# Performance work log

Hardware: AMD Instinct MI355X
Metric: run time of the kernel (lower is better)

The kernel has to match this reference:

```python
import jax, jax.numpy as jnp
import numpy as np

NUM_ENTITIES = 64
PAD, BOS, EOS = 0, 1, 2
B, S = 512, 512


def setup_inputs() -> dict:
    key = jax.random.key(0)
    k1, k2, k3 = jax.random.split(key, 3)
    emissions = jax.random.normal(k1, (B, S, NUM_ENTITIES), dtype=jnp.float32)
    entities = jax.random.randint(k2, (B, S), 0, NUM_ENTITIES)
    mask = jnp.ones((B, S), dtype=bool)
    # transitions param, initialized as in _init_transitions
    t = jax.random.uniform(k3, (NUM_ENTITIES, NUM_ENTITIES), jnp.float32, -0.1, 0.1)
    t = t.at[:, BOS].set(-10000.0)
    t = t.at[EOS, :].set(-10000.0)
    t = t.at[PAD, :].set(-10000.0)
    t = t.at[:, PAD].set(-10000.0)
    t = t.at[PAD, PAD].set(0.0)
    t = t.at[PAD, EOS].set(0.0)
    return {"emissions": emissions, "transitions": t, "entities": entities, "mask": mask}


def _crf_nll(emissions, transitions, entities, mask):
    mf = mask.astype(emissions.dtype)  # [B,S]
    # ---- gold path score (vectorized over time) ----
    first = entities[:, 0]
    last_idx = jnp.sum(mask.astype(jnp.int32), axis=1) - 1  # [B]
    last = jnp.take_along_axis(entities, last_idx[:, None], axis=1)[:, 0]
    e = jnp.take_along_axis(emissions, entities[:, :, None], axis=2)[:, :, 0]  # [B,S]
    t = transitions[entities[:, :-1], entities[:, 1:]]  # [B,S-1]
    score = (transitions[BOS, first] + e[:, 0]
             + jnp.sum((e[:, 1:] + t) * mf[:, 1:], axis=1)
             + transitions[last, EOS])  # [B]
    # ---- log partition via scan over time ----
    alpha0 = transitions[BOS][None, :] + emissions[:, 0]  # [B,E]

    def step(alpha, xs):
        em_t, m_t = xs  # [B,E], [B] bool
        # scores[b, prev, cur] = alpha[b,prev] + T[prev,cur] + em[b,cur]
        scores = alpha[:, :, None] + transitions[None, :, :] + em_t[:, None, :]
        new_alpha = jax.nn.logsumexp(scores, axis=1)  # [B,E]
        alpha = jnp.where(m_t[:, None], new_alpha, alpha)
        return alpha, None

    alpha, _ = jax.lax.scan(step, alpha0,
                            (jnp.swapaxes(emissions[:, 1:], 0, 1), mask[:, 1:].T))
    log_z = jax.nn.logsumexp(alpha + transitions[:, EOS][None, :], axis=1)  # [B]
    return -jnp.mean(score - log_z)


def reference(emissions, transitions, entities, mask):
    return _crf_nll(emissions, transitions, entities, mask)
```

## Files before the change

kernel.cpp:

```cpp
#include <hip/hip_runtime.h>

#define NE 64
#define BB 512
#define SS 512
#define TMID 256
#define NBWD (SS - 1 - TMID)
#define NCHAIN 32
#define BOS_S 1
#define EOS_S 2
#define LN2 0.69314718055994531f
#define DR 8

typedef float f32x4 __attribute__((ext_vector_type(4)));
typedef int   i32x4 __attribute__((ext_vector_type(4)));
typedef short bf16x8 __attribute__((ext_vector_type(8)));

#define WG_SCOPE __HIP_MEMORY_SCOPE_WORKGROUP

__device__ __forceinline__ float wave_sum(float v) {
#pragma unroll
    for (int off = 32; off > 0; off >>= 1)
        v += __shfl_xor(v, off, 64);
    return v;
}

__device__ __forceinline__ unsigned pack2(float lo, float hi) {
    return __builtin_amdgcn_perm(__float_as_uint(hi), __float_as_uint(lo), 0x07060302u);
}

__device__ __forceinline__ unsigned short bf16_rne(float f) {
    unsigned u = __float_as_uint(f);
    return (unsigned short)((u + 0x7fffu + ((u >> 16) & 1u)) >> 16);
}

template <bool FWD>
__device__ __forceinline__ void producer_loop(const float* embase, float (*ring)[1024],
                                              int* ready, int* cons, int p, int lane,
                                              int tmax) {
    int t = 1 + p;
    f32x4 buf[4];
    if (t <= tmax) {
        const float* r = embase + (size_t)(FWD ? t : (SS - t)) * NE;
#pragma unroll
        for (int m = 0; m < 4; ++m) buf[m] = *(const f32x4*)(r + 16 * m);
    }
    while (t <= tmax) {
        int tn = t + 3;
        f32x4 nb[4];
        if (tn <= tmax) {
            const float* r = embase + (size_t)(FWD ? tn : (SS - tn)) * NE;
#pragma unroll
            for (int m = 0; m < 4; ++m) nb[m] = *(const f32x4*)(r + 16 * m);
        }
        while (__hip_atomic_load(cons, __ATOMIC_ACQUIRE, WG_SCOPE) < t - DR)
            __builtin_amdgcn_s_sleep(1);
        int slot = t & (DR - 1);
        f32x4* dst = (f32x4*)ring[slot];
#pragma unroll
        for (int m = 0; m < 4; ++m) {
            f32x4 w;
#pragma unroll
            for (int r2 = 0; r2 < 4; ++r2) w[r2] = __expf(buf[m][r2]);
            dst[m * 64 + lane] = w;
        }
        __hip_atomic_store(&ready[slot], t, __ATOMIC_RELEASE, WG_SCOPE);
#pragma unroll
        for (int m = 0; m < 4; ++m) buf[m] = nb[m];
        t = tn;
    }
}

__global__ __launch_bounds__(512, 1) void crf_fused(const float* __restrict__ em,
                                                    const float* __restrict__ T,
                                                    const int* __restrict__ ent,
                                                    float* __restrict__ out_mean) {
    const int lane = threadIdx.x & 63;
    const int wv = threadIdx.x >> 6;

    if (blockIdx.x >= NCHAIN) {
        const int b = (blockIdx.x - NCHAIN) * 8 + wv;
        const float* emb = em + (size_t)b * SS * NE;
        const int* entb = ent + b * SS;
        float sc = 0.f;
        for (int t = lane; t < SS; t += 64) {
            int et = entb[t];
            sc += emb[t * NE + et];
            sc += (t == 0) ? T[BOS_S * NE + et] : T[entb[t - 1] * NE + et];
            if (t == SS - 1) sc += T[et * NE + EOS_S];
        }
        sc = wave_sum(sc);
        if (lane == 0) atomicAdd(out_mean, -sc * (1.0f / (float)BB));
        return;
    }

    __shared__ float ringf[DR][1024];
    __shared__ float ringb[DR][1024];
    __shared__ int readyf[DR], readyb[DR];
    __shared__ int consf, consb;
    __shared__ float wbuf[1024];
    __shared__ int shiftb_s;
    __shared__ int doneb;

    if (threadIdx.x < DR) { readyf[threadIdx.x] = 0; readyb[threadIdx.x] = 0; }
    if (threadIdx.x == 0) { consf = 0; consb = 0; doneb = 0; }
    __syncthreads();

    const int g = blockIdx.x;
    const int n = lane & 15;
    const int q = lane >> 4;

    if (wv >= 2) {
        const float* embase = em + ((size_t)(g * 16 + n) * SS) * NE + 4 * q;
        if (wv <= 4)
            producer_loop<true>(embase, ringf, readyf, &consf, wv - 2, lane, TMID);
        else
            producer_loop<false>(embase, ringb, readyb, &consb, wv - 5, lane, NBWD);
        return;
    }

#define LOAD_G(RING, READY, BUF, T_)                                             \
    do {                                                                         \
        int _slot = (T_) & (DR - 1);                                             \
        while (__hip_atomic_load(&READY[_slot], __ATOMIC_ACQUIRE, WG_SCOPE) != (T_)) {} \
        const f32x4* _src = (const f32x4*)RING[_slot];                           \
        BUF[0] = _src[0 * 64 + lane];                                            \
        BUF[1] = _src[1 * 64 + lane];                                            \
        BUF[2] = _src[2 * 64 + lane];                                            \
        BUF[3] = _src[3 * 64 + lane];                                            \
    } while (0)

#define STEP_F(T_, GCUR, GNXT, DO_LOAD)                                          \
    do {                                                                         \
        if (DO_LOAD) LOAD_G(ringf, readyf, GNXT, (T_) + 1);                      \
        unsigned u3 = (unsigned)__builtin_amdgcn_readlane(__float_as_int(d[3]), 0); \
        int kk = (int)((u3 >> 23) & 255u) - 127;                                 \
        shift += kk;                                                             \
        float scale = __uint_as_float((unsigned)(127 - kk) << 23);               \
        float ds[16];                                                            \
        _Pragma("unroll") for (int v = 0; v < 16; ++v) ds[v] = d[v] * scale;     \
        i32x4 bi0, bi1;                                                          \
        bi0[0] = (int)pack2(ds[0], ds[1]);   bi0[1] = (int)pack2(ds[2], ds[3]);  \
        bi0[2] = (int)pack2(ds[4], ds[5]);   bi0[3] = (int)pack2(ds[6], ds[7]);  \
        bi1[0] = (int)pack2(ds[8], ds[9]);   bi1[1] = (int)pack2(ds[10], ds[11]);\
        bi1[2] = (int)pack2(ds[12], ds[13]); bi1[3] = (int)pack2(ds[14], ds[15]);\
        bf16x8 B0 = __builtin_bit_cast(bf16x8, bi0);                             \
        bf16x8 B1 = __builtin_bit_cast(bf16x8, bi1);                             \
        _Pragma("unroll") for (int tm = 0; tm < 4; ++tm) {                       \
            f32x4 acc = {0.f, 0.f, 0.f, 0.f};                                    \
            acc = __builtin_amdgcn_mfma_f32_16x16x32_bf16(A[tm][0], B0, acc, 0, 0, 0); \
            acc = __builtin_amdgcn_mfma_f32_16x16x32_bf16(A[tm][1], B1, acc, 0, 0, 0); \
            _Pragma("unroll") for (int r = 0; r < 4; ++r)                        \
                d[4 * tm + r] = acc[r] * GCUR[tm][r];                            \
        }                                                                        \
        asm volatile("" ::: "memory");      \
        if (lane == 0) __hip_atomic_store(&consf, (T_), __ATOMIC_RELAXED, WG_SCOPE); \
    } while (0)

#define STEP_B(T_, GCUR, GNXT, DO_LOAD)                                          \
    do {                                                                         \
        if (DO_LOAD) LOAD_G(ringb, readyb, GNXT, (T_) + 1);                      \
        unsigned u3 = (unsigned)__builtin_amdgcn_readlane(__float_as_int(d[3]), 0); \
        int kk = (int)((u3 >> 23) & 255u) - 127;                                 \
        shift += kk;                                                             \
        float scale = __uint_as_float((unsigned)(127 - kk) << 23);               \
        float ds[16];                                                            \
        _Pragma("unroll") for (int v = 0; v < 16; ++v)                           \
            ds[v] = (d[v] * GCUR[v >> 2][v & 3]) * scale;                        \
        i32x4 bi0, bi1;                                                          \
        bi0[0] = (int)pack2(ds[0], ds[1]);   bi0[1] = (int)pack2(ds[2], ds[3]);  \
        bi0[2] = (int)pack2(ds[4], ds[5]);   bi0[3] = (int)pack2(ds[6], ds[7]);  \
        bi1[0] = (int)pack2(ds[8], ds[9]);   bi1[1] = (int)pack2(ds[10], ds[11]);\
        bi1[2] = (int)pack2(ds[12], ds[13]); bi1[3] = (int)pack2(ds[14], ds[15]);\
        bf16x8 B0 = __builtin_bit_cast(bf16x8, bi0);                             \
        bf16x8 B1 = __builtin_bit_cast(bf16x8, bi1);                             \
        _Pragma("unroll") for (int tm = 0; tm < 4; ++tm) {                       \
            f32x4 acc = {0.f, 0.f, 0.f, 0.f};                                    \
            acc = __builtin_amdgcn_mfma_f32_16x16x32_bf16(A[tm][0], B0, acc, 0, 0, 0); \
            acc = __builtin_amdgcn_mfma_f32_16x16x32_bf16(A[tm][1], B1, acc, 0, 0, 0); \
            _Pragma("unroll") for (int r = 0; r < 4; ++r)                        \
                d[4 * tm + r] = acc[r];                                          \
        }                                                                        \
        asm volatile("" ::: "memory");                                           \
        if (lane == 0) __hip_atomic_store(&consb, (T_), __ATOMIC_RELAXED, WG_SCOPE); \
    } while (0)

    if (wv == 0) {
        const int b = g * 16 + n;

        bf16x8 A[4][2];
#pragma unroll
        for (int tm = 0; tm < 4; ++tm)
#pragma unroll
            for (int kt = 0; kt < 2; ++kt) {
                i32x4 w;
#pragma unroll
                for (int pp = 0; pp < 4; ++pp) {
                    int j0 = 2 * pp, j1 = 2 * pp + 1;
                    int s0 = 16 * (2 * kt + (j0 >> 2)) + 4 * q + (j0 & 3);
                    int s1 = 16 * (2 * kt + (j1 >> 2)) + 4 * q + (j1 & 3);
                    int m = 16 * tm + n;
                    unsigned lo = bf16_rne(__expf(T[s0 * NE + m]));
                    unsigned hi = bf16_rne(__expf(T[s1 * NE + m]));
                    w[pp] = (int)(lo | (hi << 16));
                }
                A[tm][kt] = __builtin_bit_cast(bf16x8, w);
            }

        const float* pe = em + (size_t)b * SS * NE + 4 * q;
        float d[16];
        {
            f32x4 e0[4];
#pragma unroll
            for (int m = 0; m < 4; ++m) e0[m] = *(const f32x4*)(pe + 16 * m);
#pragma unroll
            for (int v = 0; v < 16; ++v) {
                int s = 16 * (v >> 2) + 4 * q + (v & 3);
                d[v] = __expf(T[BOS_S * NE + s] + e0[v >> 2][v & 3]);
            }
        }

        int shift = 0;
        f32x4 GA[4], GB[4];
        LOAD_G(ringf, readyf, GA, 1);
        for (int t = 1; t + 1 <= TMID; t += 2) {
            STEP_F(t, GA, GB, 1);
            STEP_F(t + 1, GB, GA, (t + 2 <= TMID));
        }

        while (__hip_atomic_load(&doneb, __ATOMIC_ACQUIRE, WG_SCOPE) == 0) {}
        int sb = shiftb_s;
        const float* wp = wbuf + n * 64 + q * 16;
        float partial = 0.f;
#pragma unroll
        for (int v = 0; v < 16; ++v) partial = fmaf(d[v], wp[v], partial);
        partial += __shfl_xor(partial, 16, 64);
        partial += __shfl_xor(partial, 32, 64);

        float log_z = (float)(shift + sb) * LN2 + __logf(partial);
        float val = (lane < 16) ? log_z * (1.0f / (float)BB) : 0.f;
        val = wave_sum(val);
        if (lane == 0) atomicAdd(out_mean, val);
        return;
    }

    {
        bf16x8 A[4][2];
#pragma unroll
        for (int tm = 0; tm < 4; ++tm)
#pragma unroll
            for (int kt = 0; kt < 2; ++kt) {
                i32x4 w;
#pragma unroll
                for (int pp = 0; pp < 4; ++pp) {
                    int j0 = 2 * pp, j1 = 2 * pp + 1;
                    int s0 = 16 * (2 * kt + (j0 >> 2)) + 4 * q + (j0 & 3);
                    int s1 = 16 * (2 * kt + (j1 >> 2)) + 4 * q + (j1 & 3);
                    int m = 16 * tm + n;
                    unsigned lo = bf16_rne(__expf(T[m * NE + s0]));
                    unsigned hi = bf16_rne(__expf(T[m * NE + s1]));
                    w[pp] = (int)(lo | (hi << 16));
                }
                A[tm][kt] = __builtin_bit_cast(bf16x8, w);
            }

        float d[16];
#pragma unroll
        for (int v = 0; v < 16; ++v) {
            int s = 16 * (v >> 2) + 4 * q + (v & 3);
            d[v] = __expf(T[s * NE + EOS_S]);
        }

        int shift = 0;
        f32x4 GA[4], GB[4];
        LOAD_G(ringb, readyb, GA, 1);
        int vt = 1;
        for (; vt + 1 <= NBWD; vt += 2) {
            STEP_B(vt, GA, GB, 1);
            STEP_B(vt + 1, GB, GA, (vt + 2 <= NBWD));
        }
        STEP_B(vt, GA, GB, 0);

        float* wp = wbuf + n * 64 + q * 16;
#pragma unroll
        for (int v = 0; v < 16; ++v) wp[v] = d[v];
        if (lane == 0) {
            shiftb_s = shift;
            __hip_atomic_store(&doneb, 1, __ATOMIC_RELEASE, WG_SCOPE);
        }
        return;
    }
#undef STEP_F
#undef STEP_B
#undef LOAD_G
}

extern "C" void kernel_launch(void* const* d_in, const int* in_sizes, int n_in,
                              void* d_out, int out_size, void* d_ws, size_t ws_size,
                              hipStream_t stream) {
    const float* emissions   = (const float*)d_in[0];
    const float* transitions = (const float*)d_in[1];
    const int*   entities    = (const int*)d_in[2];

    hipMemsetAsync(d_out, 0, sizeof(float), stream);
    crf_fused<<<NCHAIN + BB / 8, 512, 0, stream>>>(emissions, transitions, entities,
                                                   (float*)d_out);
}
```

Measured before the change: 79.60 us.

## Deepen producer prefetch and trim per-step sync and normalisation in CRF chains

```diff
diff --git a/kernel.cpp b/kernel.cpp
--- a/kernel.cpp
+++ b/kernel.cpp
@@ -38,17 +38,22 @@
                                               int* ready, int* cons, int p, int lane,
                                               int tmax) {
     int t = 1 + p;
-    f32x4 buf[4];
+    f32x4 b0[4], b1[4];
     if (t <= tmax) {
         const float* r = embase + (size_t)(FWD ? t : (SS - t)) * NE;
 #pragma unroll
-        for (int m = 0; m < 4; ++m) buf[m] = *(const f32x4*)(r + 16 * m);
+        for (int m = 0; m < 4; ++m) b0[m] = *(const f32x4*)(r + 16 * m);
+    }
+    if (t + 3 <= tmax) {
+        const float* r = embase + (size_t)(FWD ? (t + 3) : (SS - t - 3)) * NE;
+#pragma unroll
+        for (int m = 0; m < 4; ++m) b1[m] = *(const f32x4*)(r + 16 * m);
     }
     while (t <= tmax) {
-        int tn = t + 3;
+        int tn2 = t + 6;
         f32x4 nb[4];
-        if (tn <= tmax) {
-            const float* r = embase + (size_t)(FWD ? tn : (SS - tn)) * NE;
+        if (tn2 <= tmax) {
+            const float* r = embase + (size_t)(FWD ? tn2 : (SS - tn2)) * NE;
 #pragma unroll
             for (int m = 0; m < 4; ++m) nb[m] = *(const f32x4*)(r + 16 * m);
         }
@@ -60,13 +65,13 @@
         for (int m = 0; m < 4; ++m) {
             f32x4 w;
 #pragma unroll
-            for (int r2 = 0; r2 < 4; ++r2) w[r2] = __expf(buf[m][r2]);
+            for (int r2 = 0; r2 < 4; ++r2) w[r2] = __expf(b0[m][r2]);
             dst[m * 64 + lane] = w;
         }
         __hip_atomic_store(&ready[slot], t, __ATOMIC_RELEASE, WG_SCOPE);
 #pragma unroll
-        for (int m = 0; m < 4; ++m) buf[m] = nb[m];
-        t = tn;
+        for (int m = 0; m < 4; ++m) { b0[m] = b1[m]; b1[m] = nb[m]; }
+        t += 3;
     }
 }
 
@@ -118,26 +123,45 @@
         return;
     }
 
-#define LOAD_G(RING, READY, BUF, T_)                                             \
+#define PIPE_FLAGS(RING, READY, T_, GNXT, DO_LOAD)                               \
     do {                                                                         \
-        int _slot = (T_) & (DR - 1);                                             \
-        while (__hip_atomic_load(&READY[_slot], __ATOMIC_ACQUIRE, WG_SCOPE) != (T_)) {} \
-        const f32x4* _src = (const f32x4*)RING[_slot];                           \
-        BUF[0] = _src[0 * 64 + lane];                                            \
-        BUF[1] = _src[1 * 64 + lane];                                            \
-        BUF[2] = _src[2 * 64 + lane];                                            \
-        BUF[3] = _src[3 * 64 + lane];                                            \
+        int _fprev = fnext;                                                      \
+        fnext = __hip_atomic_load(&READY[((T_) + 2) & (DR - 1)],                 \
+                                  __ATOMIC_RELAXED, WG_SCOPE);                   \
+        if (DO_LOAD) {                                                           \
+            if (__builtin_expect(_fprev != (T_) + 1, 0)) {                       \
+                while (__hip_atomic_load(&READY[((T_) + 1) & (DR - 1)],          \
+                                         __ATOMIC_ACQUIRE, WG_SCOPE) != (T_) + 1) {} \
+            }                                                                    \
+            const f32x4* _src = (const f32x4*)RING[((T_) + 1) & (DR - 1)];       \
+            GNXT[0] = _src[0 * 64 + lane];                                       \
+            GNXT[1] = _src[1 * 64 + lane];                                       \
+            GNXT[2] = _src[2 * 64 + lane];                                       \
+            GNXT[3] = _src[3 * 64 + lane];                                       \
+        }                                                                        \
     } while (0)
 
-#define STEP_F(T_, GCUR, GNXT, DO_LOAD)                                          \
+#define CONS_STORE(CONS, T_)                                                     \
     do {                                                                         \
-        if (DO_LOAD) LOAD_G(ringf, readyf, GNXT, (T_) + 1);                      \
-        unsigned u3 = (unsigned)__builtin_amdgcn_readlane(__float_as_int(d[3]), 0); \
-        int kk = (int)((u3 >> 23) & 255u) - 127;                                 \
-        shift += kk;                                                             \
-        float scale = __uint_as_float((unsigned)(127 - kk) << 23);               \
+        asm volatile("" ::: "memory");      \
+        if ((((T_) & 1) == 0) && lane == 0)                                      \
+            __hip_atomic_store(&CONS, (T_), __ATOMIC_RELAXED, WG_SCOPE);         \
+    } while (0)
+
+
+#define STEP_F(T_, GCUR, GNXT, DO_LOAD, DO_NORM)                                 \
+    do {                                                                         \
+        PIPE_FLAGS(ringf, readyf, T_, GNXT, DO_LOAD);                            \
         float ds[16];                                                            \
-        _Pragma("unroll") for (int v = 0; v < 16; ++v) ds[v] = d[v] * scale;     \
+        if (DO_NORM) {                                                           \
+            unsigned u3 = (unsigned)__builtin_amdgcn_readlane(__float_as_int(d[3]), 0); \
+            int kk = (int)((u3 >> 23) & 255u) - 127;                             \
+            shift += kk;                                                         \
+            float scale = __uint_as_float((unsigned)(127 - kk) << 23);           \
+            _Pragma("unroll") for (int v = 0; v < 16; ++v) ds[v] = d[v] * scale; \
+        } else {                                                                 \
+            _Pragma("unroll") for (int v = 0; v < 16; ++v) ds[v] = d[v];         \
+        }                                                                        \
         i32x4 bi0, bi1;                                                          \
         bi0[0] = (int)pack2(ds[0], ds[1]);   bi0[1] = (int)pack2(ds[2], ds[3]);  \
         bi0[2] = (int)pack2(ds[4], ds[5]);   bi0[3] = (int)pack2(ds[6], ds[7]);  \
@@ -146,26 +170,30 @@
         bf16x8 B0 = __builtin_bit_cast(bf16x8, bi0);                             \
         bf16x8 B1 = __builtin_bit_cast(bf16x8, bi1);                             \
         _Pragma("unroll") for (int tm = 0; tm < 4; ++tm) {                       \
-            f32x4 acc = {0.f, 0.f, 0.f, 0.f};                                    \
-            acc = __builtin_amdgcn_mfma_f32_16x16x32_bf16(A[tm][0], B0, acc, 0, 0, 0); \
-            acc = __builtin_amdgcn_mfma_f32_16x16x32_bf16(A[tm][1], B1, acc, 0, 0, 0); \
+            f32x4 z4 = {0.f, 0.f, 0.f, 0.f};                                     \
+            f32x4 acc0 = __builtin_amdgcn_mfma_f32_16x16x32_bf16(A[tm][0], B0, z4, 0, 0, 0); \
+            f32x4 acc1 = __builtin_amdgcn_mfma_f32_16x16x32_bf16(A[tm][1], B1, z4, 0, 0, 0); \
             _Pragma("unroll") for (int r = 0; r < 4; ++r)                        \
-                d[4 * tm + r] = acc[r] * GCUR[tm][r];                            \
-        }                                                                        \
-        asm volatile("" ::: "memory");      \
-        if (lane == 0) __hip_atomic_store(&consf, (T_), __ATOMIC_RELAXED, WG_SCOPE); \
+                d[4 * tm + r] = (acc0[r] + acc1[r]) * GCUR[tm][r];               \
+        }                                                                        \
+        CONS_STORE(consf, T_);                                                   \
     } while (0)
 
-#define STEP_B(T_, GCUR, GNXT, DO_LOAD)                                          \
+#define STEP_B(T_, GCUR, GNXT, DO_LOAD, DO_NORM)                                 \
     do {                                                                         \
-        if (DO_LOAD) LOAD_G(ringb, readyb, GNXT, (T_) + 1);                      \
-        unsigned u3 = (unsigned)__builtin_amdgcn_readlane(__float_as_int(d[3]), 0); \
-        int kk = (int)((u3 >> 23) & 255u) - 127;                                 \
-        shift += kk;                                                             \
-        float scale = __uint_as_float((unsigned)(127 - kk) << 23);               \
+        PIPE_FLAGS(ringb, readyb, T_, GNXT, DO_LOAD);                            \
         float ds[16];                                                            \
-        _Pragma("unroll") for (int v = 0; v < 16; ++v)                           \
-            ds[v] = (d[v] * GCUR[v >> 2][v & 3]) * scale;                        \
+        if (DO_NORM) {                                                           \
+            unsigned u3 = (unsigned)__builtin_amdgcn_readlane(__float_as_int(d[3]), 0); \
+            int kk = (int)((u3 >> 23) & 255u) - 127;                             \
+            shift += kk;                                                         \
+            float scale = __uint_as_float((unsigned)(127 - kk) << 23);           \
+            _Pragma("unroll") for (int v = 0; v < 16; ++v)                       \
+                ds[v] = (d[v] * GCUR[v >> 2][v & 3]) * scale;                    \
+        } else {                                                                 \
+            _Pragma("unroll") for (int v = 0; v < 16; ++v)                       \
+                ds[v] = d[v] * GCUR[v >> 2][v & 3];                              \
+        }                                                                        \
         i32x4 bi0, bi1;                                                          \
         bi0[0] = (int)pack2(ds[0], ds[1]);   bi0[1] = (int)pack2(ds[2], ds[3]);  \
         bi0[2] = (int)pack2(ds[4], ds[5]);   bi0[3] = (int)pack2(ds[6], ds[7]);  \
@@ -174,17 +202,17 @@
         bf16x8 B0 = __builtin_bit_cast(bf16x8, bi0);                             \
         bf16x8 B1 = __builtin_bit_cast(bf16x8, bi1);                             \
         _Pragma("unroll") for (int tm = 0; tm < 4; ++tm) {                       \
-            f32x4 acc = {0.f, 0.f, 0.f, 0.f};                                    \
-            acc = __builtin_amdgcn_mfma_f32_16x16x32_bf16(A[tm][0], B0, acc, 0, 0, 0); \
-            acc = __builtin_amdgcn_mfma_f32_16x16x32_bf16(A[tm][1], B1, acc, 0, 0, 0); \
+            f32x4 z4 = {0.f, 0.f, 0.f, 0.f};                                     \
+            f32x4 acc0 = __builtin_amdgcn_mfma_f32_16x16x32_bf16(A[tm][0], B0, z4, 0, 0, 0); \
+            f32x4 acc1 = __builtin_amdgcn_mfma_f32_16x16x32_bf16(A[tm][1], B1, z4, 0, 0, 0); \
             _Pragma("unroll") for (int r = 0; r < 4; ++r)                        \
-                d[4 * tm + r] = acc[r];                                          \
-        }                                                                        \
-        asm volatile("" ::: "memory");                                           \
-        if (lane == 0) __hip_atomic_store(&consb, (T_), __ATOMIC_RELAXED, WG_SCOPE); \
+                d[4 * tm + r] = acc0[r] + acc1[r];                               \
+        }                                                                        \
+        CONS_STORE(consb, T_);                                                   \
     } while (0)
 
     if (wv == 0) {
+        __builtin_amdgcn_s_setprio(1);
         const int b = g * 16 + n;
 
         bf16x8 A[4][2];
@@ -221,11 +249,25 @@
 
         int shift = 0;
         f32x4 GA[4], GB[4];
-        LOAD_G(ringf, readyf, GA, 1);
-        for (int t = 1; t + 1 <= TMID; t += 2) {
-            STEP_F(t, GA, GB, 1);
-            STEP_F(t + 1, GB, GA, (t + 2 <= TMID));
-        }
+        while (__hip_atomic_load(&readyf[1], __ATOMIC_ACQUIRE, WG_SCOPE) != 1) {}
+        {
+            const f32x4* _src = (const f32x4*)ringf[1];
+            GA[0] = _src[0 * 64 + lane]; GA[1] = _src[1 * 64 + lane];
+            GA[2] = _src[2 * 64 + lane]; GA[3] = _src[3 * 64 + lane];
+        }
+        int fnext = __hip_atomic_load(&readyf[2], __ATOMIC_RELAXED, WG_SCOPE);
+
+        int t = 1;
+        for (; t + 4 <= TMID; t += 4) {
+            STEP_F(t,     GA, GB, 1, 1);
+            STEP_F(t + 1, GB, GA, 1, 0);
+            STEP_F(t + 2, GA, GB, 1, 0);
+            STEP_F(t + 3, GB, GA, 1, 0);
+        }
+        STEP_F(t,     GA, GB, 1, 1);
+        STEP_F(t + 1, GB, GA, 1, 0);
+        STEP_F(t + 2, GA, GB, 1, 0);
+        STEP_F(t + 3, GB, GA, 0, 0);
 
         while (__hip_atomic_load(&doneb, __ATOMIC_ACQUIRE, WG_SCOPE) == 0) {}
         int sb = shiftb_s;
@@ -244,6 +286,7 @@
     }
 
     {
+        __builtin_amdgcn_s_setprio(1);
         bf16x8 A[4][2];
 #pragma unroll
         for (int tm = 0; tm < 4; ++tm)
@@ -272,13 +315,24 @@
 
         int shift = 0;
         f32x4 GA[4], GB[4];
-        LOAD_G(ringb, readyb, GA, 1);
+        while (__hip_atomic_load(&readyb[1], __ATOMIC_ACQUIRE, WG_SCOPE) != 1) {}
+        {
+            const f32x4* _src = (const f32x4*)ringb[1];
+            GA[0] = _src[0 * 64 + lane]; GA[1] = _src[1 * 64 + lane];
+            GA[2] = _src[2 * 64 + lane]; GA[3] = _src[3 * 64 + lane];
+        }
+        int fnext = __hip_atomic_load(&readyb[2], __ATOMIC_RELAXED, WG_SCOPE);
+
         int vt = 1;
-        for (; vt + 1 <= NBWD; vt += 2) {
-            STEP_B(vt, GA, GB, 1);
-            STEP_B(vt + 1, GB, GA, (vt + 2 <= NBWD));
-        }
-        STEP_B(vt, GA, GB, 0);
+        for (; vt + 4 <= NBWD; vt += 4) {
+            STEP_B(vt,     GA, GB, 1, 1);
+            STEP_B(vt + 1, GB, GA, 1, 0);
+            STEP_B(vt + 2, GA, GB, 1, 0);
+            STEP_B(vt + 3, GB, GA, 1, 0);
+        }
+        STEP_B(vt,     GA, GB, 1, 1);
+        STEP_B(vt + 1, GB, GA, 1, 0);
+        STEP_B(vt + 2, GA, GB, 0, 0);
 
         float* wp = wbuf + n * 64 + q * 16;
 #pragma unroll
@@ -291,7 +345,8 @@
     }
 #undef STEP_F
 #undef STEP_B
-#undef LOAD_G
+#undef PIPE_FLAGS
+#undef CONS_STORE
 }
 
 extern "C" void kernel_launch(void* const* d_in, const int* in_sizes, int n_in,
```

Measured after the change: 81.06 us. Within noise of the previous version (+1.8%).

## Replace LDS producer ring with in-register 8-deep prefetch in chain waves

Applied to the files above, without the earlier changes.

```diff
diff --git a/kernel.cpp b/kernel.cpp
--- a/kernel.cpp
+++ b/kernel.cpp
@@ -9,7 +9,6 @@
 #define BOS_S 1
 #define EOS_S 2
 #define LN2 0.69314718055994531f
-#define DR 8
 
 typedef float f32x4 __attribute__((ext_vector_type(4)));
 typedef int   i32x4 __attribute__((ext_vector_type(4)));
@@ -33,44 +32,7 @@
     return (unsigned short)((u + 0x7fffu + ((u >> 16) & 1u)) >> 16);
 }
 
-template <bool FWD>
-__device__ __forceinline__ void producer_loop(const float* embase, float (*ring)[1024],
-                                              int* ready, int* cons, int p, int lane,
-                                              int tmax) {
-    int t = 1 + p;
-    f32x4 buf[4];
-    if (t <= tmax) {
-        const float* r = embase + (size_t)(FWD ? t : (SS - t)) * NE;
-#pragma unroll
-        for (int m = 0; m < 4; ++m) buf[m] = *(const f32x4*)(r + 16 * m);
-    }
-    while (t <= tmax) {
-        int tn = t + 3;
-        f32x4 nb[4];
-        if (tn <= tmax) {
-            const float* r = embase + (size_t)(FWD ? tn : (SS - tn)) * NE;
-#pragma unroll
-            for (int m = 0; m < 4; ++m) nb[m] = *(const f32x4*)(r + 16 * m);
-        }
-        while (__hip_atomic_load(cons, __ATOMIC_ACQUIRE, WG_SCOPE) < t - DR)
-            __builtin_amdgcn_s_sleep(1);
-        int slot = t & (DR - 1);
-        f32x4* dst = (f32x4*)ring[slot];
-#pragma unroll
-        for (int m = 0; m < 4; ++m) {
-            f32x4 w;
-#pragma unroll
-            for (int r2 = 0; r2 < 4; ++r2) w[r2] = __expf(buf[m][r2]);
-            dst[m * 64 + lane] = w;
-        }
-        __hip_atomic_store(&ready[slot], t, __ATOMIC_RELEASE, WG_SCOPE);
-#pragma unroll
-        for (int m = 0; m < 4; ++m) buf[m] = nb[m];
-        t = tn;
-    }
-}
-
-__global__ __launch_bounds__(512, 1) void crf_fused(const float* __restrict__ em,
+__global__ __launch_bounds__(256, 1) void crf_fused(const float* __restrict__ em,
                                                     const float* __restrict__ T,
                                                     const int* __restrict__ ent,
                                                     float* __restrict__ out_mean) {
@@ -78,7 +40,7 @@
     const int wv = threadIdx.x >> 6;
 
     if (blockIdx.x >= NCHAIN) {
-        const int b = (blockIdx.x - NCHAIN) * 8 + wv;
+        const int b = (blockIdx.x - NCHAIN) * 4 + wv;
         const float* emb = em + (size_t)b * SS * NE;
         const int* entb = ent + b * SS;
         float sc = 0.f;
@@ -93,100 +55,38 @@
         return;
     }
 
-    __shared__ float ringf[DR][1024];
-    __shared__ float ringb[DR][1024];
-    __shared__ int readyf[DR], readyb[DR];
-    __shared__ int consf, consb;
     __shared__ float wbuf[1024];
     __shared__ int shiftb_s;
     __shared__ int doneb;
 
-    if (threadIdx.x < DR) { readyf[threadIdx.x] = 0; readyb[threadIdx.x] = 0; }
-    if (threadIdx.x == 0) { consf = 0; consb = 0; doneb = 0; }
+    if (threadIdx.x == 0) doneb = 0;
     __syncthreads();
+    if (wv >= 2) return;
 
     const int g = blockIdx.x;
     const int n = lane & 15;
     const int q = lane >> 4;
-
-    if (wv >= 2) {
-        const float* embase = em + ((size_t)(g * 16 + n) * SS) * NE + 4 * q;
-        if (wv <= 4)
-            producer_loop<true>(embase, ringf, readyf, &consf, wv - 2, lane, TMID);
-        else
-            producer_loop<false>(embase, ringb, readyb, &consb, wv - 5, lane, NBWD);
-        return;
-    }
-
-#define LOAD_G(RING, READY, BUF, T_)                                             \
-    do {                                                                         \
-        int _slot = (T_) & (DR - 1);                                             \
-        while (__hip_atomic_load(&READY[_slot], __ATOMIC_ACQUIRE, WG_SCOPE) != (T_)) {} \
-        const f32x4* _src = (const f32x4*)RING[_slot];                           \
-        BUF[0] = _src[0 * 64 + lane];                                            \
-        BUF[1] = _src[1 * 64 + lane];                                            \
-        BUF[2] = _src[2 * 64 + lane];                                            \
-        BUF[3] = _src[3 * 64 + lane];                                            \
-    } while (0)
-
-#define STEP_F(T_, GCUR, GNXT, DO_LOAD)                                          \
-    do {                                                                         \
-        if (DO_LOAD) LOAD_G(ringf, readyf, GNXT, (T_) + 1);                      \
-        unsigned u3 = (unsigned)__builtin_amdgcn_readlane(__float_as_int(d[3]), 0); \
-        int kk = (int)((u3 >> 23) & 255u) - 127;                                 \
-        shift += kk;                                                             \
-        float scale = __uint_as_float((unsigned)(127 - kk) << 23);               \
-        float ds[16];                                                            \
-        _Pragma("unroll") for (int v = 0; v < 16; ++v) ds[v] = d[v] * scale;     \
+    const int b = g * 16 + n;
+    const float* pe = em + (size_t)b * SS * NE + 4 * q;
+
+
+#define PACK_DS()                                                                \
         i32x4 bi0, bi1;                                                          \
         bi0[0] = (int)pack2(ds[0], ds[1]);   bi0[1] = (int)pack2(ds[2], ds[3]);  \
         bi0[2] = (int)pack2(ds[4], ds[5]);   bi0[3] = (int)pack2(ds[6], ds[7]);  \
         bi1[0] = (int)pack2(ds[8], ds[9]);   bi1[1] = (int)pack2(ds[10], ds[11]);\
         bi1[2] = (int)pack2(ds[12], ds[13]); bi1[3] = (int)pack2(ds[14], ds[15]);\
         bf16x8 B0 = __builtin_bit_cast(bf16x8, bi0);                             \
-        bf16x8 B1 = __builtin_bit_cast(bf16x8, bi1);                             \
-        _Pragma("unroll") for (int tm = 0; tm < 4; ++tm) {                       \
-            f32x4 acc = {0.f, 0.f, 0.f, 0.f};                                    \
-            acc = __builtin_amdgcn_mfma_f32_16x16x32_bf16(A[tm][0], B0, acc, 0, 0, 0); \
-            acc = __builtin_amdgcn_mfma_f32_16x16x32_bf16(A[tm][1], B1, acc, 0, 0, 0); \
-            _Pragma("unroll") for (int r = 0; r < 4; ++r)                        \
-                d[4 * tm + r] = acc[r] * GCUR[tm][r];                            \
-        }                                                                        \
-        asm volatile("" ::: "memory");      \
-        if (lane == 0) __hip_atomic_store(&consf, (T_), __ATOMIC_RELAXED, WG_SCOPE); \
-    } while (0)
-
-#define STEP_B(T_, GCUR, GNXT, DO_LOAD)                                          \
-    do {                                                                         \
-        if (DO_LOAD) LOAD_G(ringb, readyb, GNXT, (T_) + 1);                      \
+        bf16x8 B1 = __builtin_bit_cast(bf16x8, bi1)
+
+#define DO_NORM_DS(PRE)                                                          \
         unsigned u3 = (unsigned)__builtin_amdgcn_readlane(__float_as_int(d[3]), 0); \
         int kk = (int)((u3 >> 23) & 255u) - 127;                                 \
         shift += kk;                                                             \
         float scale = __uint_as_float((unsigned)(127 - kk) << 23);               \
-        float ds[16];                                                            \
-        _Pragma("unroll") for (int v = 0; v < 16; ++v)                           \
-            ds[v] = (d[v] * GCUR[v >> 2][v & 3]) * scale;                        \
-        i32x4 bi0, bi1;                                                          \
-        bi0[0] = (int)pack2(ds[0], ds[1]);   bi0[1] = (int)pack2(ds[2], ds[3]);  \
-        bi0[2] = (int)pack2(ds[4], ds[5]);   bi0[3] = (int)pack2(ds[6], ds[7]);  \
-        bi1[0] = (int)pack2(ds[8], ds[9]);   bi1[1] = (int)pack2(ds[10], ds[11]);\
-        bi1[2] = (int)pack2(ds[12], ds[13]); bi1[3] = (int)pack2(ds[14], ds[15]);\
-        bf16x8 B0 = __builtin_bit_cast(bf16x8, bi0);                             \
-        bf16x8 B1 = __builtin_bit_cast(bf16x8, bi1);                             \
-        _Pragma("unroll") for (int tm = 0; tm < 4; ++tm) {                       \
-            f32x4 acc = {0.f, 0.f, 0.f, 0.f};                                    \
-            acc = __builtin_amdgcn_mfma_f32_16x16x32_bf16(A[tm][0], B0, acc, 0, 0, 0); \
-            acc = __builtin_amdgcn_mfma_f32_16x16x32_bf16(A[tm][1], B1, acc, 0, 0, 0); \
-            _Pragma("unroll") for (int r = 0; r < 4; ++r)                        \
-                d[4 * tm + r] = acc[r];                                          \
-        }                                                                        \
-        asm volatile("" ::: "memory");                                           \
-        if (lane == 0) __hip_atomic_store(&consb, (T_), __ATOMIC_RELAXED, WG_SCOPE); \
-    } while (0)
+        _Pragma("unroll") for (int v = 0; v < 16; ++v) ds[v] = (PRE) * scale
 
     if (wv == 0) {
-        const int b = g * 16 + n;
-
         bf16x8 A[4][2];
 #pragma unroll
         for (int tm = 0; tm < 4; ++tm)
@@ -206,7 +106,6 @@
                 A[tm][kt] = __builtin_bit_cast(bf16x8, w);
             }
 
-        const float* pe = em + (size_t)b * SS * NE + 4 * q;
         float d[16];
         {
             f32x4 e0[4];
@@ -219,12 +118,45 @@
             }
         }
 
+        f32x4 RAW[8][4];
+#pragma unroll
+        for (int j = 0; j < 8; ++j)
+#pragma unroll
+            for (int m = 0; m < 4; ++m)
+                RAW[j][m] = *(const f32x4*)(pe + (size_t)(1 + j) * NE + 16 * m);
+
         int shift = 0;
-        f32x4 GA[4], GB[4];
-        LOAD_G(ringf, readyf, GA, 1);
-        for (int t = 1; t + 1 <= TMID; t += 2) {
-            STEP_F(t, GA, GB, 1);
-            STEP_F(t + 1, GB, GA, (t + 2 <= TMID));
+        for (int tb = 1; tb <= TMID; tb += 8) {
+#pragma unroll
+            for (int j = 0; j < 8; ++j) {
+                float GE[16];
+#pragma unroll
+                for (int m = 0; m < 4; ++m)
+#pragma unroll
+                    for (int r = 0; r < 4; ++r)
+                        GE[4 * m + r] = __expf(RAW[j][m][r]);
+#pragma unroll
+                for (int m = 0; m < 4; ++m)
+                    RAW[j][m] = *(const f32x4*)(pe + (size_t)(tb + j + 8) * NE + 16 * m);
+
+                float ds[16];
+                if ((j & 3) == 0) {
+                    DO_NORM_DS(d[v]);
+                } else {
+#pragma unroll
+                    for (int v = 0; v < 16; ++v) ds[v] = d[v];
+                }
+                PACK_DS();
+#pragma unroll
+                for (int tm = 0; tm < 4; ++tm) {
+                    f32x4 acc = {0.f, 0.f, 0.f, 0.f};
+                    acc = __builtin_amdgcn_mfma_f32_16x16x32_bf16(A[tm][0], B0, acc, 0, 0, 0);
+                    acc = __builtin_amdgcn_mfma_f32_16x16x32_bf16(A[tm][1], B1, acc, 0, 0, 0);
+#pragma unroll
+                    for (int r = 0; r < 4; ++r)
+                        d[4 * tm + r] = acc[r] * GE[4 * tm + r];
+                }
+            }
         }
 
         while (__hip_atomic_load(&doneb, __ATOMIC_ACQUIRE, WG_SCOPE) == 0) {}
@@ -270,15 +202,54 @@
             d[v] = __expf(T[s * NE + EOS_S]);
         }
 
+        f32x4 RAW[8][4];
+#pragma unroll
+        for (int j = 0; j < 8; ++j)
+#pragma unroll
+            for (int m = 0; m < 4; ++m)
+                RAW[j][m] = *(const f32x4*)(pe + (size_t)(SS - 1 - j) * NE + 16 * m);
+
         int shift = 0;
-        f32x4 GA[4], GB[4];
-        LOAD_G(ringb, readyb, GA, 1);
-        int vt = 1;
-        for (; vt + 1 <= NBWD; vt += 2) {
-            STEP_B(vt, GA, GB, 1);
-            STEP_B(vt + 1, GB, GA, (vt + 2 <= NBWD));
-        }
-        STEP_B(vt, GA, GB, 0);
+
+#define BWD_STEP(J, VT, DO_LOAD, NORM)                                           \
+    do {                                                                         \
+        float GE[16];                                                            \
+        _Pragma("unroll") for (int m = 0; m < 4; ++m)                            \
+            _Pragma("unroll") for (int r = 0; r < 4; ++r)                        \
+                GE[4 * m + r] = __expf(RAW[J][m][r]);                            \
+        if (DO_LOAD) {                                                           \
+            _Pragma("unroll") for (int m = 0; m < 4; ++m)                        \
+                RAW[J][m] = *(const f32x4*)(pe + (size_t)(SS - ((VT) + 8)) * NE + 16 * m); \
+        }                                                                        \
+        float ds[16];                                                            \
+        if (NORM) {                                                              \
+            DO_NORM_DS(d[v] * GE[v]);                                            \
+        } else {                                                                 \
+            _Pragma("unroll") for (int v = 0; v < 16; ++v) ds[v] = d[v] * GE[v]; \
+        }                                                                        \
+        PACK_DS();                                                               \
+        _Pragma("unroll") for (int tm = 0; tm < 4; ++tm) {                       \
+            f32x4 acc = {0.f, 0.f, 0.f, 0.f};                                    \
+            acc = __builtin_amdgcn_mfma_f32_16x16x32_bf16(A[tm][0], B0, acc, 0, 0, 0); \
+            acc = __builtin_amdgcn_mfma_f32_16x16x32_bf16(A[tm][1], B1, acc, 0, 0, 0); \
+            _Pragma("unroll") for (int r = 0; r < 4; ++r)                        \
+                d[4 * tm + r] = acc[r];                                          \
+        }                                                                        \
+    } while (0)
+
+        for (int vtb = 1; vtb <= NBWD - 14; vtb += 8) {
+#pragma unroll
+            for (int j = 0; j < 8; ++j)
+                BWD_STEP(j, vtb + j, 1, ((j & 3) == 0));
+        }
+        BWD_STEP(0, 249, 0, 1);
+        BWD_STEP(1, 250, 0, 0);
+        BWD_STEP(2, 251, 0, 0);
+        BWD_STEP(3, 252, 0, 0);
+        BWD_STEP(4, 253, 0, 1);
+        BWD_STEP(5, 254, 0, 0);
+        BWD_STEP(6, 255, 0, 0);
+#undef BWD_STEP
 
         float* wp = wbuf + n * 64 + q * 16;
 #pragma unroll
@@ -289,9 +260,8 @@
         }
         return;
     }
-#undef STEP_F
-#undef STEP_B
-#undef LOAD_G
+#undef PACK_DS
+#undef DO_NORM_DS
 }
 
 extern "C" void kernel_launch(void* const* d_in, const int* in_sizes, int n_in,
@@ -302,6 +272,6 @@
     const int*   entities    = (const int*)d_in[2];
 
     hipMemsetAsync(d_out, 0, sizeof(float), stream);
-    crf_fused<<<NCHAIN + BB / 8, 512, 0, stream>>>(emissions, transitions, entities,
+    crf_fused<<<NCHAIN + BB / 4, 256, 0, stream>>>(emissions, transitions, entities,
                                                    (float*)d_out);
 }
```

Result: faster. 77.56 us (-2.6%).
